# Kernel optimization log

Hardware: AMD Instinct MI355X
Metric: run time of the kernel (lower is better)

## Reference

```python
import jax, jax.numpy as jnp
import numpy as np

V = 10000
E = 60000
B = 8
LATENT = 512
HIDDEN = 256
NUM_LAYERS = 5


def setup_inputs() -> dict:
    key = jax.random.key(0)
    ks = jax.random.split(key, 12)
    vertex_xyz = jax.random.normal(ks[0], (V, 3), dtype=jnp.float32)
    latent = jax.random.normal(ks[1], (B, LATENT), dtype=jnp.float32)
    edge_index = jax.random.randint(ks[2], (2, E), 0, V, dtype=jnp.int64)
    s = 0.02
    input_W = jax.random.normal(ks[3], (HIDDEN, LATENT + 3), dtype=jnp.float32) * s
    input_b = jnp.zeros((HIDDEN,), dtype=jnp.float32)
    conv_W = jax.random.normal(ks[4], (NUM_LAYERS, HIDDEN, HIDDEN), dtype=jnp.float32) * s
    conv_b = jnp.zeros((NUM_LAYERS, HIDDEN), dtype=jnp.float32)
    out_W = jax.random.normal(ks[5], (3, HIDDEN), dtype=jnp.float32) * s
    out_b = jnp.zeros((3,), dtype=jnp.float32)
    return dict(vertex_xyz=vertex_xyz, latent=latent, edge_index=edge_index,
                input_W=input_W, input_b=input_b, conv_W=conv_W, conv_b=conv_b,
                out_W=out_W, out_b=out_b)


def _gcn_norm(edge_index, num_nodes):
    # PyG GCNConv default: add self-loops, symmetric normalization.
    src, dst = edge_index[0], edge_index[1]
    loop = jnp.arange(num_nodes, dtype=src.dtype)
    src = jnp.concatenate([src, loop])
    dst = jnp.concatenate([dst, loop])
    deg = jax.ops.segment_sum(jnp.ones_like(dst, dtype=jnp.float32), dst,
                              num_segments=num_nodes)
    dinv = jnp.where(deg > 0, jax.lax.rsqrt(deg), 0.0)
    norm = dinv[src] * dinv[dst]  # [E+V]
    return src, dst, norm


def reference(vertex_xyz, latent, edge_index, input_W, input_b, conv_W, conv_b, out_W, out_b):
    Bn, Vn = latent.shape[0], vertex_xyz.shape[0]
    # Build node features: concat template xyz with broadcast latent -> [B, V, 3+latent]
    x = jnp.concatenate([
        jnp.broadcast_to(vertex_xyz[None], (Bn, Vn, 3)),
        jnp.broadcast_to(latent[:, None, :], (Bn, Vn, latent.shape[1])),
    ], axis=-1)
    x = jax.nn.relu(jnp.einsum('bvf,hf->bvh', x, input_W) + input_b)

    # The batched edge_index is a per-graph copy offset by b*V, so normalization
    # and message passing are identical per batch; vectorize over B.
    src, dst, norm = _gcn_norm(edge_index, Vn)
    for l in range(conv_W.shape[0]):
        h = jnp.einsum('bvh,oh->bvo', x, conv_W[l])        # linear transform
        msg = h[:, src, :] * norm[None, :, None]           # gather + scale
        agg = jnp.zeros_like(h).at[:, dst, :].add(msg)     # scatter-add
        x = jax.nn.relu(agg + conv_b[l])

    disp = jnp.einsum('bvh,oh->bvo', x, out_W) + out_b     # [B, V, 3]
    return disp
```

## Files before the change

### kernel.cpp

```cpp
#include <hip/hip_runtime.h>

#define Vn 10000
#define En 60000
#define Bb 8
#define LAT 512
#define HID 256
#define NL 5
#define Mrows (Bb * Vn)

typedef __attribute__((ext_vector_type(4))) int    i32x4;
typedef __attribute__((ext_vector_type(4))) float  f32x4;
typedef __attribute__((ext_vector_type(8))) short  bf16x8;
typedef __attribute__((ext_vector_type(4))) unsigned short u16x4;

__device__ __forceinline__ float bf2f(unsigned short u) {
    union { unsigned int u; float f; } c;
    c.u = ((unsigned int)u) << 16;
    return c.f;
}
__device__ __forceinline__ unsigned short f2bf(float f) {
    union { float f; unsigned int u; } c;
    c.f = f;
    unsigned int u = c.u + 0x7FFFu + ((c.u >> 16) & 1u);
    return (unsigned short)(u >> 16);
}


__global__ void k_init(int* cnt, int* cur) {
    int i = blockIdx.x * blockDim.x + threadIdx.x;
    if (i < Vn) { cnt[i] = 0; cur[i] = 0; }
}

__global__ void k_count(const int* __restrict__ dst, int* __restrict__ cnt) {
    int e = blockIdx.x * blockDim.x + threadIdx.x;
    if (e < En) atomicAdd(&cnt[dst[e]], 1);
}

__global__ void k_dinv(const int* __restrict__ cnt, float* __restrict__ dinv,
                       float* __restrict__ selfn) {
    int v = blockIdx.x * blockDim.x + threadIdx.x;
    if (v < Vn) {
        float d = (float)cnt[v] + 1.0f;
        float r = rsqrtf(d);
        dinv[v] = r;
        selfn[v] = r * r;
    }
}

__global__ void k_scan(const int* __restrict__ cnt, int* __restrict__ rowptr) {
    __shared__ int part[1024];
    const int PER = 10;
    int tid = threadIdx.x;
    int base = tid * PER;
    int local[PER];
    int s = 0;
#pragma unroll
    for (int i = 0; i < PER; ++i) {
        int idx = base + i;
        int c = (idx < Vn) ? cnt[idx] : 0;
        local[i] = s;
        s += c;
    }
    part[tid] = s;
    __syncthreads();
    for (int off = 1; off < 1024; off <<= 1) {
        int add = (tid >= off) ? part[tid - off] : 0;
        __syncthreads();
        part[tid] += add;
        __syncthreads();
    }
    int chunk_base = part[tid] - s;
#pragma unroll
    for (int i = 0; i < PER; ++i) {
        int idx = base + i;
        if (idx < Vn) rowptr[idx] = chunk_base + local[i];
    }
    if (tid == 1023) rowptr[Vn] = part[1023];
}

__global__ void k_fill(const int* __restrict__ src, const int* __restrict__ dst,
                       const float* __restrict__ dinv, const int* __restrict__ rowptr,
                       int* __restrict__ cur, int* __restrict__ csr_src,
                       float* __restrict__ csr_norm) {
    int e = blockIdx.x * blockDim.x + threadIdx.x;
    if (e < En) {
        int s = src[e], d = dst[e];
        int p = atomicAdd(&cur[d], 1);
        int idx = rowptr[d] + p;
        csr_src[idx] = s;
        csr_norm[idx] = dinv[s] * dinv[d];
    }
}


__global__ void k_wcvt(const float* __restrict__ W, unsigned short* __restrict__ Wb, int n) {
    int i = blockIdx.x * blockDim.x + threadIdx.x;
    if (i < n) Wb[i] = f2bf(W[i]);
}


__global__ __launch_bounds__(256) void k_latc(const float* __restrict__ latent,
                                              const float* __restrict__ input_W,
                                              const float* __restrict__ input_b,
                                              float* __restrict__ latc,
                                              float* __restrict__ w3p) {
    int gid = blockIdx.x * 256 + threadIdx.x;
    int q = gid & 3;
    int i = gid >> 2;
    int b = i >> 8, h = i & 255;
    const float* wr = input_W + (size_t)h * (LAT + 3) + 3 + q * 128;
    const float* lr = latent + (size_t)b * LAT + q * 128;
    float s = 0.0f;
#pragma unroll 8
    for (int k = 0; k < 128; ++k) s = fmaf(lr[k], wr[k], s);
    s += __shfl_xor(s, 1, 64);
    s += __shfl_xor(s, 2, 64);
    if (q == 0) latc[i] = s + input_b[h];
    if (gid < 768) w3p[gid] = input_W[(size_t)(gid & 255) * (LAT + 3) + (gid >> 8)];
}

__global__ __launch_bounds__(256) void k_input(const float* __restrict__ xyz,
                                               const float* __restrict__ w3p,
                                               const float* __restrict__ latc,
                                               unsigned short* __restrict__ X) {
    int gid = blockIdx.x * 256 + threadIdx.x;
    int row = gid >> 5;
    int hc = (gid & 31) << 3;
    int b = row / Vn;
    int v = row - b * Vn;
    float x0 = xyz[v * 3 + 0], x1 = xyz[v * 3 + 1], x2 = xyz[v * 3 + 2];
    const float* lc = latc + b * HID + hc;
    u16x4 o0, o1;
#pragma unroll
    for (int j = 0; j < 8; ++j) {
        float s = lc[j];
        s = fmaf(x0, w3p[hc + j], s);
        s = fmaf(x1, w3p[256 + hc + j], s);
        s = fmaf(x2, w3p[512 + hc + j], s);
        unsigned short r = f2bf(fmaxf(s, 0.0f));
        if (j < 4) o0[j] = r; else o1[j - 4] = r;
    }
    u16x4* dst = (u16x4*)&X[(size_t)row * HID + hc];
    dst[0] = o0;
    dst[1] = o1;
}


__global__ __launch_bounds__(256) void k_agg(const unsigned short* __restrict__ Xin,
                                             unsigned short* __restrict__ Xa,
                                             const int* __restrict__ rowptr,
                                             const int* __restrict__ csr_src,
                                             const float* __restrict__ csr_norm,
                                             const float* __restrict__ selfn) {
    int wid = threadIdx.x >> 6;
    int lane = threadIdx.x & 63;
    int bv = blockIdx.x * 4 + wid;
    int b = bv / Vn;
    int v = bv - b * Vn;
    int f = lane << 2;
    size_t bbase = (size_t)b * Vn * HID;

    u16x4 hs = *(const u16x4*)&Xin[(size_t)bv * HID + f];
    float sn = selfn[v];
    float a0 = sn * bf2f(hs[0]), a1 = sn * bf2f(hs[1]);
    float a2 = sn * bf2f(hs[2]), a3 = sn * bf2f(hs[3]);

    int s = rowptr[v], e = rowptr[v + 1];
    int i = s;
    for (; i + 2 <= e; i += 2) {
        float n0 = csr_norm[i], n1 = csr_norm[i + 1];
        int s0 = csr_src[i], s1 = csr_src[i + 1];
        u16x4 h0 = *(const u16x4*)&Xin[bbase + (size_t)s0 * HID + f];
        u16x4 h1 = *(const u16x4*)&Xin[bbase + (size_t)s1 * HID + f];
        a0 = fmaf(n0, bf2f(h0[0]), a0); a1 = fmaf(n0, bf2f(h0[1]), a1);
        a2 = fmaf(n0, bf2f(h0[2]), a2); a3 = fmaf(n0, bf2f(h0[3]), a3);
        a0 = fmaf(n1, bf2f(h1[0]), a0); a1 = fmaf(n1, bf2f(h1[1]), a1);
        a2 = fmaf(n1, bf2f(h1[2]), a2); a3 = fmaf(n1, bf2f(h1[3]), a3);
    }
    if (i < e) {
        float n0 = csr_norm[i];
        u16x4 h0 = *(const u16x4*)&Xin[bbase + (size_t)csr_src[i] * HID + f];
        a0 = fmaf(n0, bf2f(h0[0]), a0); a1 = fmaf(n0, bf2f(h0[1]), a1);
        a2 = fmaf(n0, bf2f(h0[2]), a2); a3 = fmaf(n0, bf2f(h0[3]), a3);
    }
    u16x4 r;
    r[0] = f2bf(a0); r[1] = f2bf(a1); r[2] = f2bf(a2); r[3] = f2bf(a3);
    *(u16x4*)&Xa[(size_t)bv * HID + f] = r;
}


__global__ __launch_bounds__(256) void k_gemm(const unsigned short* __restrict__ A,
                                              const unsigned short* __restrict__ Wb,
                                              const float* __restrict__ bias,
                                              unsigned short* __restrict__ Xout) {
    __shared__ __align__(16) char smem[32768];
    const int t = threadIdx.x;
    const int w = t >> 6;
    const int l = t & 63;
    const int m0 = blockIdx.x * 64;
    const int n0w = w * 64;
    const int lr = l & 15;
    const int lg = l >> 4;

    bf16x8 Bf[4][8];
#pragma unroll
    for (int nt = 0; nt < 4; ++nt) {
        const unsigned short* wp = Wb + (size_t)(n0w + nt * 16 + lr) * HID + lg * 8;
#pragma unroll
        for (int ks = 0; ks < 8; ++ks)
            Bf[nt][ks] = __builtin_bit_cast(bf16x8, *(const i32x4*)(wp + ks * 32));
    }

    {
        const char* src = (const char*)(A + (size_t)m0 * HID);
#pragma unroll
        for (int i = 0; i < 8; ++i) {
            int x = i * 4096 + t * 16;
            i32x4 v = *(const i32x4*)(src + x);
            int sw = (x & ~511) | ((x & 511) ^ (((x >> 9) & 7) << 4));
            *(i32x4*)(smem + sw) = v;
        }
    }
    __syncthreads();

    f32x4 acc[4][4];
#pragma unroll
    for (int mt = 0; mt < 4; ++mt)
#pragma unroll
        for (int nt = 0; nt < 4; ++nt)
            acc[mt][nt] = (f32x4){0.f, 0.f, 0.f, 0.f};

#pragma unroll
    for (int ks = 0; ks < 8; ++ks) {
#pragma unroll
        for (int mt = 0; mt < 4; ++mt) {
            int row = mt * 16 + lr;
            int colb = ks * 64 + lg * 16;
            int addr = row * 512 + (colb ^ ((row & 7) << 4));
            bf16x8 a = __builtin_bit_cast(bf16x8, *(const i32x4*)(smem + addr));
#pragma unroll
            for (int nt = 0; nt < 4; ++nt)
                acc[mt][nt] = __builtin_amdgcn_mfma_f32_16x16x32_bf16(
                    a, Bf[nt][ks], acc[mt][nt], 0, 0, 0);
        }
    }

    __syncthreads();

    float bnt[4];
#pragma unroll
    for (int nt = 0; nt < 4; ++nt) bnt[nt] = bias[n0w + nt * 16 + lr];

#pragma unroll
    for (int mt = 0; mt < 4; ++mt)
#pragma unroll
        for (int nt = 0; nt < 4; ++nt)
#pragma unroll
            for (int r = 0; r < 4; ++r) {
                int row = mt * 16 + lg * 4 + r;
                int col = n0w + nt * 16 + lr;
                float vv = fmaxf(acc[mt][nt][r] + bnt[nt], 0.0f);
                int addr = row * 512 + (((col * 2) & 511) ^ ((row & 7) << 4));
                *(unsigned short*)(smem + addr) = f2bf(vv);
            }
    __syncthreads();

    char* dstb = (char*)(Xout + (size_t)m0 * HID);
#pragma unroll
    for (int i = 0; i < 8; ++i) {
        int x = i * 4096 + t * 16;
        int sw = (x & ~511) | ((x & 511) ^ (((x >> 9) & 7) << 4));
        *(i32x4*)(dstb + x) = *(const i32x4*)(smem + sw);
    }
}


__global__ __launch_bounds__(256) void k_out(const unsigned short* __restrict__ X,
                                             const float* __restrict__ oW,
                                             const float* __restrict__ ob,
                                             float* __restrict__ disp) {
    int wid = threadIdx.x >> 6;
    int lane = threadIdx.x & 63;
    int bv = blockIdx.x * 4 + wid;
    int f = lane << 2;
    u16x4 xv = *(const u16x4*)&X[(size_t)bv * HID + f];
    float x0 = bf2f(xv[0]), x1 = bf2f(xv[1]), x2 = bf2f(xv[2]), x3 = bf2f(xv[3]);
    float p[3];
#pragma unroll
    for (int c = 0; c < 3; ++c) {
        f32x4 wv = *(const f32x4*)&oW[c * HID + f];
        p[c] = x0 * wv[0] + x1 * wv[1] + x2 * wv[2] + x3 * wv[3];
    }
#pragma unroll
    for (int off = 32; off > 0; off >>= 1) {
#pragma unroll
        for (int c = 0; c < 3; ++c) p[c] += __shfl_down(p[c], off, 64);
    }
    if (lane == 0) {
#pragma unroll
        for (int c = 0; c < 3; ++c) disp[(size_t)bv * 3 + c] = p[c] + ob[c];
    }
}


extern "C" void kernel_launch(void* const* d_in, const int* in_sizes, int n_in,
                              void* d_out, int out_size, void* d_ws, size_t ws_size,
                              hipStream_t stream) {
    const float* xyz     = (const float*)d_in[0];
    const float* latent  = (const float*)d_in[1];
    const int*   eidx    = (const int*)d_in[2];
    const float* input_W = (const float*)d_in[3];
    const float* input_b = (const float*)d_in[4];
    const float* conv_W  = (const float*)d_in[5];
    const float* conv_b  = (const float*)d_in[6];
    const float* out_W   = (const float*)d_in[7];
    const float* out_b   = (const float*)d_in[8];
    float* disp = (float*)d_out;

    const int* src = eidx;
    const int* dst = eidx + En;

    char* base = (char*)d_ws;
    size_t off = 0;
    auto alloc = [&](size_t bytes) {
        size_t o = off;
        off = (off + bytes + 255) & ~(size_t)255;
        return (void*)(base + o);
    };
    int*   cnt      = (int*)alloc(Vn * 4);
    int*   cur      = (int*)alloc(Vn * 4);
    float* dinv     = (float*)alloc(Vn * 4);
    float* selfn    = (float*)alloc(Vn * 4);
    int*   rowptr   = (int*)alloc((Vn + 1) * 4);
    int*   csr_src  = (int*)alloc(En * 4);
    float* csr_norm = (float*)alloc(En * 4);
    float* latc     = (float*)alloc(Bb * HID * 4);
    float* w3p      = (float*)alloc(3 * HID * 4);
    unsigned short* Wb = (unsigned short*)alloc((size_t)NL * HID * HID * 2);
    unsigned short* X  = (unsigned short*)alloc((size_t)Mrows * HID * 2);
    unsigned short* Xa = (unsigned short*)alloc((size_t)Mrows * HID * 2);

    k_init<<<(Vn + 255) / 256, 256, 0, stream>>>(cnt, cur);
    k_count<<<(En + 255) / 256, 256, 0, stream>>>(dst, cnt);
    k_dinv<<<(Vn + 255) / 256, 256, 0, stream>>>(cnt, dinv, selfn);
    k_scan<<<1, 1024, 0, stream>>>(cnt, rowptr);
    k_fill<<<(En + 255) / 256, 256, 0, stream>>>(src, dst, dinv, rowptr, cur, csr_src, csr_norm);

    k_wcvt<<<(NL * HID * HID + 255) / 256, 256, 0, stream>>>(conv_W, Wb, NL * HID * HID);

    k_latc<<<32, 256, 0, stream>>>(latent, input_W, input_b, latc, w3p);
    k_input<<<Mrows * 32 / 256, 256, 0, stream>>>(xyz, w3p, latc, X);

    for (int l = 0; l < NL; ++l) {
        k_agg<<<Mrows / 4, 256, 0, stream>>>(X, Xa, rowptr, csr_src, csr_norm, selfn);
        k_gemm<<<Mrows / 64, 256, 0, stream>>>(Xa, Wb + (size_t)l * HID * HID,
                                               conv_b + (size_t)l * HID, X);
    }

    k_out<<<Mrows / 4, 256, 0, stream>>>(X, out_W, out_b, disp);
}
```

Baseline: 514.1 us.

## Merge setup kernels and rework GEMM loads, swizzle and epilogue stores

Folds the degree-normalisation kernel into the scan kernel and the weight-conversion kernel into the latent-projection kernel, which removes two launches. In the GEMM, the A-tile global loads are issued into registers before the weight-fragment loads so their latency overlaps, and the LDS swizzle widens from 8 to 16 rows. The MFMA operands are swapped so each lane holds four consecutive output columns, letting the epilogue use vectorised bias loads and 8-byte LDS stores instead of scalar 2-byte ones. The cost is a longer serial loop in the single-block scan and higher register pressure from staging the A tile in registers.

```diff
diff --git a/kernel.cpp b/kernel.cpp
--- a/kernel.cpp
+++ b/kernel.cpp
@@ -36,18 +36,8 @@
     if (e < En) atomicAdd(&cnt[dst[e]], 1);
 }
 
-__global__ void k_dinv(const int* __restrict__ cnt, float* __restrict__ dinv,
-                       float* __restrict__ selfn) {
-    int v = blockIdx.x * blockDim.x + threadIdx.x;
-    if (v < Vn) {
-        float d = (float)cnt[v] + 1.0f;
-        float r = rsqrtf(d);
-        dinv[v] = r;
-        selfn[v] = r * r;
-    }
-}
-
-__global__ void k_scan(const int* __restrict__ cnt, int* __restrict__ rowptr) {
+__global__ void k_scan(const int* __restrict__ cnt, int* __restrict__ rowptr,
+                       float* __restrict__ dinv, float* __restrict__ selfn) {
     __shared__ int part[1024];
     const int PER = 10;
     int tid = threadIdx.x;
@@ -58,6 +48,12 @@
     for (int i = 0; i < PER; ++i) {
         int idx = base + i;
         int c = (idx < Vn) ? cnt[idx] : 0;
+        if (idx < Vn) {
+            float d = (float)c + 1.0f;
+            float r = rsqrtf(d);
+            dinv[idx] = r;
+            selfn[idx] = r * r;
+        }
         local[i] = s;
         s += c;
     }
@@ -93,18 +89,20 @@
 }
 
 
-__global__ void k_wcvt(const float* __restrict__ W, unsigned short* __restrict__ Wb, int n) {
-    int i = blockIdx.x * blockDim.x + threadIdx.x;
-    if (i < n) Wb[i] = f2bf(W[i]);
-}
-
-
-__global__ __launch_bounds__(256) void k_latc(const float* __restrict__ latent,
+__global__ __launch_bounds__(256) void k_prep(const float* __restrict__ conv_W,
+                                              unsigned short* __restrict__ Wb,
+                                              const float* __restrict__ latent,
                                               const float* __restrict__ input_W,
                                               const float* __restrict__ input_b,
                                               float* __restrict__ latc,
                                               float* __restrict__ w3p) {
-    int gid = blockIdx.x * 256 + threadIdx.x;
+    int blk = blockIdx.x;
+    if (blk < 1280) {
+        int i = blk * 256 + threadIdx.x;
+        Wb[i] = f2bf(conv_W[i]);
+        return;
+    }
+    int gid = (blk - 1280) * 256 + threadIdx.x;
     int q = gid & 3;
     int i = gid >> 2;
     int b = i >> 8, h = i & 255;
@@ -202,6 +200,14 @@
     const int lr = l & 15;
     const int lg = l >> 4;
 
+    i32x4 av[8];
+    {
+        const char* srcb = (const char*)(A + (size_t)m0 * HID);
+#pragma unroll
+        for (int i = 0; i < 8; ++i)
+            av[i] = *(const i32x4*)(srcb + i * 4096 + t * 16);
+    }
+
     bf16x8 Bf[4][8];
 #pragma unroll
     for (int nt = 0; nt < 4; ++nt) {
@@ -211,15 +217,11 @@
             Bf[nt][ks] = __builtin_bit_cast(bf16x8, *(const i32x4*)(wp + ks * 32));
     }
 
-    {
-        const char* src = (const char*)(A + (size_t)m0 * HID);
-#pragma unroll
-        for (int i = 0; i < 8; ++i) {
-            int x = i * 4096 + t * 16;
-            i32x4 v = *(const i32x4*)(src + x);
-            int sw = (x & ~511) | ((x & 511) ^ (((x >> 9) & 7) << 4));
-            *(i32x4*)(smem + sw) = v;
-        }
+#pragma unroll
+    for (int i = 0; i < 8; ++i) {
+        int x = i * 4096 + t * 16;
+        int sw = (x & ~511) | ((x & 511) ^ (((x >> 9) & 15) << 4));
+        *(i32x4*)(smem + sw) = av[i];
     }
     __syncthreads();
 
@@ -236,40 +238,44 @@
         for (int mt = 0; mt < 4; ++mt) {
             int row = mt * 16 + lr;
             int colb = ks * 64 + lg * 16;
-            int addr = row * 512 + (colb ^ ((row & 7) << 4));
+            int addr = row * 512 + (colb ^ ((row & 15) << 4));
             bf16x8 a = __builtin_bit_cast(bf16x8, *(const i32x4*)(smem + addr));
 #pragma unroll
             for (int nt = 0; nt < 4; ++nt)
                 acc[mt][nt] = __builtin_amdgcn_mfma_f32_16x16x32_bf16(
-                    a, Bf[nt][ks], acc[mt][nt], 0, 0, 0);
+                    Bf[nt][ks], a, acc[mt][nt], 0, 0, 0);
         }
     }
 
     __syncthreads();
 
-    float bnt[4];
-#pragma unroll
-    for (int nt = 0; nt < 4; ++nt) bnt[nt] = bias[n0w + nt * 16 + lr];
-
-#pragma unroll
-    for (int mt = 0; mt < 4; ++mt)
-#pragma unroll
-        for (int nt = 0; nt < 4; ++nt)
-#pragma unroll
-            for (int r = 0; r < 4; ++r) {
-                int row = mt * 16 + lg * 4 + r;
-                int col = n0w + nt * 16 + lr;
-                float vv = fmaxf(acc[mt][nt][r] + bnt[nt], 0.0f);
-                int addr = row * 512 + (((col * 2) & 511) ^ ((row & 7) << 4));
-                *(unsigned short*)(smem + addr) = f2bf(vv);
-            }
+    f32x4 bb[4];
+#pragma unroll
+    for (int nt = 0; nt < 4; ++nt)
+        bb[nt] = *(const f32x4*)&bias[n0w + nt * 16 + lg * 4];
+
+#pragma unroll
+    for (int mt = 0; mt < 4; ++mt) {
+        int row = mt * 16 + lr;
+        int rs = (row & 15) << 4;
+#pragma unroll
+        for (int nt = 0; nt < 4; ++nt) {
+            u16x4 ov;
+#pragma unroll
+            for (int r = 0; r < 4; ++r)
+                ov[r] = f2bf(fmaxf(acc[mt][nt][r] + bb[nt][r], 0.0f));
+            int colbyte = n0w * 2 + nt * 32 + lg * 8;
+            int addr = row * 512 + (colbyte ^ rs);
+            *(u16x4*)(smem + addr) = ov;
+        }
+    }
     __syncthreads();
 
     char* dstb = (char*)(Xout + (size_t)m0 * HID);
 #pragma unroll
     for (int i = 0; i < 8; ++i) {
         int x = i * 4096 + t * 16;
-        int sw = (x & ~511) | ((x & 511) ^ (((x >> 9) & 7) << 4));
+        int sw = (x & ~511) | ((x & 511) ^ (((x >> 9) & 15) << 4));
         *(i32x4*)(dstb + x) = *(const i32x4*)(smem + sw);
     }
 }
@@ -342,13 +348,11 @@
 
     k_init<<<(Vn + 255) / 256, 256, 0, stream>>>(cnt, cur);
     k_count<<<(En + 255) / 256, 256, 0, stream>>>(dst, cnt);
-    k_dinv<<<(Vn + 255) / 256, 256, 0, stream>>>(cnt, dinv, selfn);
-    k_scan<<<1, 1024, 0, stream>>>(cnt, rowptr);
+    k_scan<<<1, 1024, 0, stream>>>(cnt, rowptr, dinv, selfn);
     k_fill<<<(En + 255) / 256, 256, 0, stream>>>(src, dst, dinv, rowptr, cur, csr_src, csr_norm);
 
-    k_wcvt<<<(NL * HID * HID + 255) / 256, 256, 0, stream>>>(conv_W, Wb, NL * HID * HID);
-
-    k_latc<<<32, 256, 0, stream>>>(latent, input_W, input_b, latc, w3p);
+    k_prep<<<1312, 256, 0, stream>>>(conv_W, Wb, latent, input_W, input_b, latc, w3p);
+
     k_input<<<Mrows * 32 / 256, 256, 0, stream>>>(xyz, w3p, latc, X);
 
     for (int l = 0; l < NL; ++l) {
```

Result: no change. 516.6 us (+0.5%).
